# Kernel tuning notes

Measured on AMD Instinct MI355X. Metric: run time of the kernel, lower is better.

The kernel has to match this reference:

```python
import jax, jax.numpy as jnp
import numpy as np

N, IN, OUT, T = 65536, 256, 256, 8


def setup_inputs() -> dict:
    key = jax.random.key(0)
    k1, k2, k3, k4 = jax.random.split(key, 4)
    x = jax.random.normal(k1, (N, IN), dtype=jnp.float32)
    types = jax.random.randint(k2, (N,), 0, T, dtype=jnp.int32)
    # xavier_uniform for W: limit = sqrt(6 / (fan_in + fan_out)) with fan computed
    # on the last two dims (out_size, in_size)
    limit = float(np.sqrt(6.0 / (IN + OUT)))
    W = jax.random.uniform(k3, (T, OUT, IN), dtype=jnp.float32, minval=-limit, maxval=limit)
    # original inits b to zeros; use small random values so the bias path is exercised
    b = 0.01 * jax.random.normal(k4, (T, OUT), dtype=jnp.float32)
    return {"x": x, "types": types, "W": W, "b": b}


def reference(x, types, W, b):
    # out[i] = W[types[i]] @ x[i] + b[types[i]]
    # Grouped-GEMM expressed as a loop over the small fixed set of types,
    # avoiding the huge [N, OUT, IN] gather of W[types].
    num_types = W.shape[0]
    out = b[types]  # [N, OUT]
    for t in range(num_types):
        mask = (types == t)[:, None]  # [N, 1]
        out = out + jnp.where(mask, x @ W[t].T, jnp.float32(0.0))
    return out
```

## Files before the change

kernel.cpp:

```cpp
#include <hip/hip_runtime.h>
#include <stdint.h>


#define NROWS 65536
#define NTYPES 8
#define KDIM 256
#define ODIM 256
#define BM 128
#define BN 128
#define BK 64
#define MAX_TILES (NROWS / BM + NTYPES - 1)

typedef __attribute__((ext_vector_type(8))) short short8;
typedef __attribute__((ext_vector_type(4))) float f32x4;

__device__ __forceinline__ unsigned short f2bf(float f) {
    unsigned int u = __float_as_uint(f);
    u += 0x7fffu + ((u >> 16) & 1u);
    return (unsigned short)(u >> 16);
}

__global__ void prep_bucket_kernel(const float* __restrict__ W,
                                   unsigned short* __restrict__ Wb,
                                   const int* __restrict__ types,
                                   int* __restrict__ cnt,
                                   int* __restrict__ idx) {
    const int b = blockIdx.x;
    if (b < 512) {
        int i = b * 256 + threadIdx.x;
        float4 v = ((const float4*)W)[i];
        ushort4 p;
        p.x = f2bf(v.x); p.y = f2bf(v.y); p.z = f2bf(v.z); p.w = f2bf(v.w);
        ((ushort4*)Wb)[i] = p;
    } else {
        __shared__ int h[NTYPES];
        __shared__ int base[NTYPES];
        int i = (b - 512) * 256 + threadIdx.x;
        if (threadIdx.x < NTYPES) h[threadIdx.x] = 0;
        __syncthreads();
        int t = types[i];
        int r = atomicAdd(&h[t], 1);
        __syncthreads();
        if (threadIdx.x < NTYPES)
            base[threadIdx.x] = atomicAdd(&cnt[threadIdx.x], h[threadIdx.x]);
        __syncthreads();
        idx[t * NROWS + base[t] + r] = i;
    }
}

__global__ __launch_bounds__(256, 4)
void gemm_kernel(const float* __restrict__ x,
                 const float* __restrict__ bias,
                 const unsigned short* __restrict__ Wb,
                 const int* __restrict__ cnt,
                 const int* __restrict__ idx,
                 float* __restrict__ out) {
    const int bid = blockIdx.x;
    int t = -1, m0 = 0, count = 0, accum = 0;
    #pragma unroll
    for (int i = 0; i < NTYPES; ++i) {
        int c = cnt[i];
        int ntile = (c + BM - 1) / BM;
        if (t < 0 && bid < accum + ntile) { t = i; m0 = (bid - accum) * BM; count = c; }
        accum += ntile;
    }
    if (t < 0) return;
    const int n0 = blockIdx.y * BN;

    __shared__ int idx_s[BM];
    __shared__ float bias_s[BN];
    __shared__ unsigned short As[BM * BK];
    __shared__ unsigned short Bs[BN * BK];

    const int tid = threadIdx.x;

    if (tid < BM) {
        int m = m0 + tid;
        idx_s[tid] = (m < count) ? idx[t * NROWS + m] : 0;
    } else {
        bias_s[tid - BM] = bias[t * ODIM + n0 + (tid - BM)];
    }
    __syncthreads();

    const int wave = tid >> 6;
    const int lane = tid & 63;
    const int lr = lane & 15;
    const int lq = lane >> 4;
    const int wm = (wave >> 1) * 64;
    const int wn = (wave & 1) * 64;

    f32x4 acc[4][4] = {};

    const int srow = tid >> 4;
    const int sc   = tid & 15;

    char* AsB = (char*)As;
    char* BsB = (char*)Bs;

    for (int k0 = 0; k0 < KDIM; k0 += BK) {
        #pragma unroll
        for (int it = 0; it < 4; ++it) {
            int dbyte = wave * 4096 + it * 1024;
            int drow  = (dbyte >> 7) + (lane >> 3);
            int schunk = (lane & 7) ^ (lane >> 3);
            const unsigned short* src =
                Wb + (size_t)(t * ODIM + n0 + drow) * KDIM + k0 + schunk * 8;
            __builtin_amdgcn_global_load_lds(
                (const __attribute__((address_space(1))) void*)src,
                (__attribute__((address_space(3))) void*)(BsB + dbyte),
                16, 0, 0);
        }
        float4 av[8];
        #pragma unroll
        for (int j = 0; j < 8; ++j) {
            int row = j * 16 + srow;
            av[j] = *(const float4*)(x + (size_t)idx_s[row] * KDIM + k0 + sc * 4);
        }
        #pragma unroll
        for (int j = 0; j < 8; ++j) {
            int row = j * 16 + srow;
            ushort4 p;
            p.x = f2bf(av[j].x); p.y = f2bf(av[j].y);
            p.z = f2bf(av[j].z); p.w = f2bf(av[j].w);
            int ch = (sc >> 1) ^ (row & 7);
            *(ushort4*)(AsB + row * 128 + ch * 16 + (sc & 1) * 8) = p;
        }
        __syncthreads();

        #pragma unroll
        for (int kh = 0; kh < 2; ++kh) {
            short8 af[4], bf[4];
            #pragma unroll
            for (int i = 0; i < 4; ++i) {
                int arow = wm + i * 16 + lr;
                int ach = ((kh << 2) + lq) ^ (arow & 7);
                af[i] = *(const short8*)(AsB + arow * 128 + ach * 16);
            }
            #pragma unroll
            for (int i = 0; i < 4; ++i) {
                int brow = wn + i * 16 + lr;
                int bch = ((kh << 2) + lq) ^ (brow & 7);
                bf[i] = *(const short8*)(BsB + brow * 128 + bch * 16);
            }
            #pragma unroll
            for (int i = 0; i < 4; ++i)
                #pragma unroll
                for (int j = 0; j < 4; ++j)
                    acc[i][j] = __builtin_amdgcn_mfma_f32_16x16x32_bf16(
                        af[i], bf[j], acc[i][j], 0, 0, 0);
        }
        __syncthreads();
    }

    #pragma unroll
    for (int i = 0; i < 4; ++i) {
        int lmBase = wm + i * 16 + lq * 4;
        #pragma unroll
        for (int r = 0; r < 4; ++r) {
            int lm = lmBase + r;
            if (m0 + lm < count) {
                size_t orow = (size_t)idx_s[lm] * ODIM;
                #pragma unroll
                for (int j = 0; j < 4; ++j) {
                    int col = wn + j * 16 + lr;
                    out[orow + n0 + col] = acc[i][j][r] + bias_s[col];
                }
            }
        }
    }
}

extern "C" void kernel_launch(void* const* d_in, const int* in_sizes, int n_in,
                              void* d_out, int out_size, void* d_ws, size_t ws_size,
                              hipStream_t stream) {
    const float* x     = (const float*)d_in[0];
    const int*   types = (const int*)d_in[1];
    const float* W     = (const float*)d_in[2];
    const float* b     = (const float*)d_in[3];
    float* out = (float*)d_out;

    char* ws = (char*)d_ws;
    int* cnt = (int*)ws;
    int* idx = (int*)(ws + 1024);
    unsigned short* Wb = (unsigned short*)(ws + 1024 + (size_t)NTYPES * NROWS * sizeof(int));

    hipMemsetAsync(cnt, 0, NTYPES * sizeof(int), stream);
    prep_bucket_kernel<<<768, 256, 0, stream>>>(W, Wb, types, cnt, idx);
    dim3 grid(MAX_TILES, ODIM / BN);
    gemm_kernel<<<grid, 256, 0, stream>>>(x, b, Wb, cnt, idx, out);
}
```

Measured before the change: 137.5 us.

## Prepack W into MFMA fragment layout and stream B directly from global

The prep kernel now writes W as bf16 in the exact per-lane MFMA fragment order, so the GEMM loads B operands straight from global/L2 into registers with no LDS staging. Each block handles 64 rows across the full 256 output columns and full K, loading its whole gathered and converted A tile into LDS once with a single barrier. This removes the per-K-step barriers and the split of N across blocks, so each gathered x row is read once instead of twice. In exchange, every block re-reads all of W[t] from cache, and there is no overlap between loads and MFMA inside the unrolled loop.

```diff
diff --git a/kernel.cpp b/kernel.cpp
--- a/kernel.cpp
+++ b/kernel.cpp
@@ -6,9 +6,7 @@
 #define NTYPES 8
 #define KDIM 256
 #define ODIM 256
-#define BM 128
-#define BN 128
-#define BK 64
+#define BM 64
 #define MAX_TILES (NROWS / BM + NTYPES - 1)
 
 typedef __attribute__((ext_vector_type(8))) short short8;
@@ -21,21 +19,31 @@
 }
 
 __global__ void prep_bucket_kernel(const float* __restrict__ W,
-                                   unsigned short* __restrict__ Wb,
+                                   unsigned short* __restrict__ Wp,
                                    const int* __restrict__ types,
                                    int* __restrict__ cnt,
                                    int* __restrict__ idx) {
     const int b = blockIdx.x;
-    if (b < 512) {
-        int i = b * 256 + threadIdx.x;
-        float4 v = ((const float4*)W)[i];
-        ushort4 p;
-        p.x = f2bf(v.x); p.y = f2bf(v.y); p.z = f2bf(v.z); p.w = f2bf(v.w);
-        ((ushort4*)Wb)[i] = p;
+    if (b < 256) {
+        const int gid = b * 256 + threadIdx.x;
+        const int t = gid >> 13;
+        const int rem = gid & 8191;
+        const int f = rem >> 9;
+        const int q = (rem >> 6) & 7;
+        const int l = rem & 63;
+        const float* src = W + ((size_t)t * ODIM + f * 16 + (l & 15)) * KDIM
+                             + q * 32 + (l >> 4) * 8;
+        const float4 v0 = *(const float4*)src;
+        const float4 v1 = *(const float4*)(src + 4);
+        ushort4 p0, p1;
+        p0.x = f2bf(v0.x); p0.y = f2bf(v0.y); p0.z = f2bf(v0.z); p0.w = f2bf(v0.w);
+        p1.x = f2bf(v1.x); p1.y = f2bf(v1.y); p1.z = f2bf(v1.z); p1.w = f2bf(v1.w);
+        ushort4* dst = (ushort4*)(Wp + (size_t)gid * 8);
+        dst[0] = p0; dst[1] = p1;
     } else {
         __shared__ int h[NTYPES];
         __shared__ int base[NTYPES];
-        int i = (b - 512) * 256 + threadIdx.x;
+        int i = (b - 256) * 256 + threadIdx.x;
         if (threadIdx.x < NTYPES) h[threadIdx.x] = 0;
         __syncthreads();
         int t = types[i];
@@ -51,7 +59,7 @@
 __global__ __launch_bounds__(256, 4)
 void gemm_kernel(const float* __restrict__ x,
                  const float* __restrict__ bias,
-                 const unsigned short* __restrict__ Wb,
+                 const unsigned short* __restrict__ Wp,
                  const int* __restrict__ cnt,
                  const int* __restrict__ idx,
                  float* __restrict__ out) {
@@ -65,20 +73,29 @@
         accum += ntile;
     }
     if (t < 0) return;
-    const int n0 = blockIdx.y * BN;
 
-    __shared__ int idx_s[BM];
-    __shared__ float bias_s[BN];
-    __shared__ unsigned short As[BM * BK];
-    __shared__ unsigned short Bs[BN * BK];
+    __shared__ unsigned short As[BM * KDIM];
+    char* AsB = (char*)As;
 
     const int tid = threadIdx.x;
+    const int srow = tid >> 4;
+    const int sc   = tid & 15;
 
-    if (tid < BM) {
-        int m = m0 + tid;
-        idx_s[tid] = (m < count) ? idx[t * NROWS + m] : 0;
-    } else {
-        bias_s[tid - BM] = bias[t * ODIM + n0 + (tid - BM)];
+    #pragma unroll
+    for (int p = 0; p < 4; ++p) {
+        const int row = p * 16 + srow;
+        const int gr = m0 + row;
+        const int xr = idx[t * NROWS + (gr < count ? gr : count - 1)];
+        const float* xs = x + (size_t)xr * KDIM;
+        #pragma unroll
+        for (int s = 0; s < 4; ++s) {
+            const int slot = s * 16 + sc;
+            const float4 v = *(const float4*)(xs + slot * 4);
+            ushort4 pk;
+            pk.x = f2bf(v.x); pk.y = f2bf(v.y); pk.z = f2bf(v.z); pk.w = f2bf(v.w);
+            const int c = slot >> 1;
+            *(ushort4*)(AsB + row * 512 + (c ^ (row & 7)) * 16 + (slot & 1) * 8) = pk;
+        }
     }
     __syncthreads();
 
@@ -86,85 +103,48 @@
     const int lane = tid & 63;
     const int lr = lane & 15;
     const int lq = lane >> 4;
-    const int wm = (wave >> 1) * 64;
-    const int wn = (wave & 1) * 64;
+
+    const unsigned short* Wpt = Wp + (size_t)t * 16 * 8 * 512;
 
     f32x4 acc[4][4] = {};
 
-    const int srow = tid >> 4;
-    const int sc   = tid & 15;
-
-    char* AsB = (char*)As;
-    char* BsB = (char*)Bs;
-
-    for (int k0 = 0; k0 < KDIM; k0 += BK) {
+    #pragma unroll
+    for (int q = 0; q < 8; ++q) {
+        short8 bf[4], af[4];
         #pragma unroll
-        for (int it = 0; it < 4; ++it) {
-            int dbyte = wave * 4096 + it * 1024;
-            int drow  = (dbyte >> 7) + (lane >> 3);
-            int schunk = (lane & 7) ^ (lane >> 3);
-            const unsigned short* src =
-                Wb + (size_t)(t * ODIM + n0 + drow) * KDIM + k0 + schunk * 8;
-            __builtin_amdgcn_global_load_lds(
-                (const __attribute__((address_space(1))) void*)src,
-                (__attribute__((address_space(3))) void*)(BsB + dbyte),
-                16, 0, 0);
-        }
-        float4 av[8];
+        for (int j = 0; j < 4; ++j)
+            bf[j] = *(const short8*)(Wpt + ((size_t)((wave * 4 + j) * 8 + q)) * 512
+                                         + lane * 8);
         #pragma unroll
-        for (int j = 0; j < 8; ++j) {
-            int row = j * 16 + srow;
-            av[j] = *(const float4*)(x + (size_t)idx_s[row] * KDIM + k0 + sc * 4);
+        for (int i = 0; i < 4; ++i) {
+            const int row = i * 16 + lr;
+            af[i] = *(const short8*)(AsB + row * 512
+                                         + (((q << 2) + lq) ^ (row & 7)) * 16);
         }
         #pragma unroll
-        for (int j = 0; j < 8; ++j) {
-            int row = j * 16 + srow;
-            ushort4 p;
-            p.x = f2bf(av[j].x); p.y = f2bf(av[j].y);
-            p.z = f2bf(av[j].z); p.w = f2bf(av[j].w);
-            int ch = (sc >> 1) ^ (row & 7);
-            *(ushort4*)(AsB + row * 128 + ch * 16 + (sc & 1) * 8) = p;
-        }
-        __syncthreads();
+        for (int i = 0; i < 4; ++i)
+            #pragma unroll
+            for (int j = 0; j < 4; ++j)
+                acc[i][j] = __builtin_amdgcn_mfma_f32_16x16x32_bf16(
+                    af[i], bf[j], acc[i][j], 0, 0, 0);
+    }
 
-        #pragma unroll
-        for (int kh = 0; kh < 2; ++kh) {
-            short8 af[4], bf[4];
-            #pragma unroll
-            for (int i = 0; i < 4; ++i) {
-                int arow = wm + i * 16 + lr;
-                int ach = ((kh << 2) + lq) ^ (arow & 7);
-                af[i] = *(const short8*)(AsB + arow * 128 + ach * 16);
-            }
-            #pragma unroll
-            for (int i = 0; i < 4; ++i) {
-                int brow = wn + i * 16 + lr;
-                int bch = ((kh << 2) + lq) ^ (brow & 7);
-                bf[i] = *(const short8*)(BsB + brow * 128 + bch * 16);
-            }
-            #pragma unroll
-            for (int i = 0; i < 4; ++i)
-                #pragma unroll
-                for (int j = 0; j < 4; ++j)
-                    acc[i][j] = __builtin_amdgcn_mfma_f32_16x16x32_bf16(
-                        af[i], bf[j], acc[i][j], 0, 0, 0);
-        }
-        __syncthreads();
-    }
+    float bv[4];
+    #pragma unroll
+    for (int j = 0; j < 4; ++j)
+        bv[j] = bias[t * ODIM + wave * 64 + j * 16 + lr];
 
     #pragma unroll
     for (int i = 0; i < 4; ++i) {
-        int lmBase = wm + i * 16 + lq * 4;
         #pragma unroll
         for (int r = 0; r < 4; ++r) {
-            int lm = lmBase + r;
-            if (m0 + lm < count) {
-                size_t orow = (size_t)idx_s[lm] * ODIM;
+            const int lm = i * 16 + lq * 4 + r;
+            const int gr = m0 + lm;
+            if (gr < count) {
+                const size_t orow = (size_t)idx[t * NROWS + gr] * ODIM;
                 #pragma unroll
-                for (int j = 0; j < 4; ++j) {
-                    int col = wn + j * 16 + lr;
-                    out[orow + n0 + col] = acc[i][j][r] + bias_s[col];
-                }
+                for (int j = 0; j < 4; ++j)
+                    out[orow + wave * 64 + j * 16 + lr] = acc[i][j][r] + bv[j];
             }
         }
     }
@@ -182,10 +162,9 @@
     char* ws = (char*)d_ws;
     int* cnt = (int*)ws;
     int* idx = (int*)(ws + 1024);
-    unsigned short* Wb = (unsigned short*)(ws + 1024 + (size_t)NTYPES * NROWS * sizeof(int));
+    unsigned short* Wp = (unsigned short*)(ws + 1024 + (size_t)NTYPES * NROWS * sizeof(int));
 
     hipMemsetAsync(cnt, 0, NTYPES * sizeof(int), stream);
-    prep_bucket_kernel<<<768, 256, 0, stream>>>(W, Wb, types, cnt, idx);
-    dim3 grid(MAX_TILES, ODIM / BN);
-    gemm_kernel<<<grid, 256, 0, stream>>>(x, b, Wb, cnt, idx, out);
+    prep_bucket_kernel<<<512, 256, 0, stream>>>(W, Wp, types, cnt, idx);
+    gemm_kernel<<<MAX_TILES, 256, 0, stream>>>(x, b, Wp, cnt, idx, out);
 }
```

Result: faster. 134.5 us (-2.2%).
